# Performance work log

Measured on AMD Instinct MI355X. Metric: run time of the kernel, lower is better.

The kernel has to match this reference:

```python
import jax, jax.numpy as jnp
import numpy as np

HIDDEN = 2048
NUM_HEADS = 16
HEAD_DIM = HIDDEN // NUM_HEADS  # 128
LAYER_IDX = 0


def setup_inputs() -> dict:
    key = jax.random.key(0)
    k1, k2, k3, k4, k5 = jax.random.split(key, 5)
    B, S = 2, 2048
    hidden_states = jax.random.normal(k1, (B, S, HIDDEN), dtype=jnp.float32)
    # causal mask, broadcastable to attn shape (B, Q, H, K)
    causal = jnp.tril(jnp.ones((S, S), dtype=jnp.bool_))  # [Q, K]
    attention_mask = causal[None, :, None, :]  # [1, Q, 1, K]
    c_attn_w = jax.random.normal(k2, (HIDDEN, HIDDEN + 2 * HEAD_DIM), dtype=jnp.float32) * 0.02
    c_attn_b = jax.random.normal(k3, (HIDDEN + 2 * HEAD_DIM,), dtype=jnp.float32) * 0.02
    c_proj_w = jax.random.normal(k4, (HIDDEN, HIDDEN), dtype=jnp.float32) * 0.02
    c_proj_b = jax.random.normal(k5, (HIDDEN,), dtype=jnp.float32) * 0.02
    return {
        "hidden_states": hidden_states,
        "attention_mask": attention_mask,
        "c_attn_w": c_attn_w,
        "c_attn_b": c_attn_b,
        "c_proj_w": c_proj_w,
        "c_proj_b": c_proj_b,
    }


def reference(hidden_states, attention_mask, c_attn_w, c_attn_b, c_proj_w, c_proj_b):
    B, S, D = hidden_states.shape
    H, hd = NUM_HEADS, HEAD_DIM
    # c_attn then split into per-head query and shared (MQA) key/value
    qkv = hidden_states @ c_attn_w + c_attn_b  # [B, S, D + 2*hd]
    query = qkv[..., :D].reshape(B, S, H, hd)  # [B, Q, H, hd]
    k = qkv[..., D:D + hd]                     # [B, K, hd] shared across heads
    v = qkv[..., D + hd:]                      # [B, K, hd]
    # fp32 input => upcast=False => unscale=1, scale = 1/sqrt(head_dim)
    scale = 1.0 / jnp.sqrt(jnp.float32(hd))
    scores = jnp.einsum('bqhd,bkd->bqhk', query, k) * scale  # [B, Q, H, K]
    mask_value = jnp.finfo(jnp.float32).min
    scores = jnp.where(attention_mask, scores, mask_value)
    attn = jax.nn.softmax(scores, axis=-1)
    attn_output = jnp.einsum('bqhk,bkd->bqhd', attn, v).reshape(B, S, D)
    attn_output = attn_output @ c_proj_w + c_proj_b
    return attn_output
```

## Files before the change

### kernel.cpp

```cpp
#include <hip/hip_runtime.h>
#include <hip/hip_bf16.h>

typedef __bf16 bf16_t;
typedef __bf16 bf16x8 __attribute__((ext_vector_type(8)));
typedef __bf16 bf16x4 __attribute__((ext_vector_type(4)));
typedef float f32x4 __attribute__((ext_vector_type(4)));

#define S_LEN 2048
#define HID   2048
#define NH    16
#define HD    128
#define QKVN  2304
#define NEG_BIG (-30000.0f)

__device__ __forceinline__ void gld_lds16(const bf16_t* g, bf16_t* l) {
  __builtin_amdgcn_global_load_lds(
      (const __attribute__((address_space(1))) void*)((const void*)g),
      (__attribute__((address_space(3))) void*)((void*)l), 16, 0, 0);
}

__global__ __launch_bounds__(256) void cvt_f32_bf16_kernel(
    const float* __restrict__ in, bf16_t* __restrict__ out, int n)
{
  int i = (blockIdx.x * 256 + threadIdx.x) * 4;
  if (i < n) {
    float4 v = *(const float4*)(in + i);
    bf16x4 o;
    o[0] = (bf16_t)v.x; o[1] = (bf16_t)v.y; o[2] = (bf16_t)v.z; o[3] = (bf16_t)v.w;
    *(bf16x4*)(out + i) = o;
  }
}

__global__ __launch_bounds__(256) void transpose_cvt_kernel(
    const float* __restrict__ in, bf16_t* __restrict__ out, int K, int N)
{
  int nc = threadIdx.x & 63;
  int kg = threadIdx.x >> 6;
  int n  = blockIdx.x * 64 + nc;
  int kb = blockIdx.y * 32 + kg * 8;
  bf16x8 v;
  #pragma unroll
  for (int i = 0; i < 8; ++i) v[i] = (bf16_t)in[(size_t)(kb + i) * N + n];
  *(bf16x8*)(out + (size_t)n * K + kb) = v;
}

__global__ __launch_bounds__(256) void vt_extract_kernel(
    const bf16_t* __restrict__ qkv, bf16_t* __restrict__ vtg)
{
  int d  = threadIdx.x & 127;
  int sg = threadIdx.x >> 7;
  int b  = blockIdx.y;
  int s8 = blockIdx.x * 2 + sg;
  bf16x8 v;
  #pragma unroll
  for (int i = 0; i < 8; ++i)
    v[i] = qkv[((size_t)(b * S_LEN + s8 * 8 + i)) * QKVN + HID + HD + d];
  *(bf16x8*)(vtg + ((size_t)(b * HD + d)) * S_LEN + s8 * 8) = v;
}

template <typename OutT>
__global__ __launch_bounds__(256) void gemm_bias_kernel(
    const bf16_t* __restrict__ A, const bf16_t* __restrict__ WT,
    const float* __restrict__ bias, OutT* __restrict__ C,
    int K, int lda, int ldc)
{
  __shared__ bf16_t Ash[128 * 64];
  __shared__ bf16_t Bsh[128 * 64];

  const int tid  = threadIdx.x;
  const int wave = tid >> 6;
  const int lane = tid & 63;
  const int quad = lane >> 4;
  const int c16  = lane & 15;
  const int wm = wave >> 1;
  const int wn = wave & 1;
  const int n0 = blockIdx.x * 128;
  const int m0 = blockIdx.y * 128;

  f32x4 acc[4][4] = {};

  for (int k0 = 0; k0 < K; k0 += 64) {
    __syncthreads();
    #pragma unroll
    for (int j = 0; j < 4; ++j) {
      int cbase = wave * 256 + j * 64;
      int c = cbase + lane;
      int row = c >> 3;
      int kcl = (c ^ row) & 7;
      gld_lds16(A  + (size_t)(m0 + row) * lda + k0 + kcl * 8, Ash + cbase * 8);
      gld_lds16(WT + (size_t)(n0 + row) * K   + k0 + kcl * 8, Bsh + cbase * 8);
    }
    __syncthreads();

    #pragma unroll
    for (int kk = 0; kk < 2; ++kk) {
      bf16x8 af[4], bfr[4];
      #pragma unroll
      for (int rb = 0; rb < 4; ++rb) {
        int row = wm * 64 + rb * 16 + c16;
        int kcp = ((kk * 4 + quad) ^ row) & 7;
        af[rb] = *(const bf16x8*)(Ash + row * 64 + kcp * 8);
      }
      #pragma unroll
      for (int nt = 0; nt < 4; ++nt) {
        int row = wn * 64 + nt * 16 + c16;
        int kcp = ((kk * 4 + quad) ^ row) & 7;
        bfr[nt] = *(const bf16x8*)(Bsh + row * 64 + kcp * 8);
      }
      #pragma unroll
      for (int rb = 0; rb < 4; ++rb)
        #pragma unroll
        for (int nt = 0; nt < 4; ++nt)
          acc[rb][nt] = __builtin_amdgcn_mfma_f32_16x16x32_bf16(af[rb], bfr[nt],
                                                                acc[rb][nt], 0, 0, 0);
    }
  }

  #pragma unroll
  for (int nt = 0; nt < 4; ++nt) {
    int col = n0 + wn * 64 + nt * 16 + c16;
    float bv = bias[col];
    #pragma unroll
    for (int rb = 0; rb < 4; ++rb) {
      int rbase = m0 + wm * 64 + rb * 16 + quad * 4;
      #pragma unroll
      for (int r = 0; r < 4; ++r)
        C[(size_t)(rbase + r) * ldc + col] = (OutT)(acc[rb][nt][r] + bv);
    }
  }
}

__global__ __launch_bounds__(512, 4) void mqa_attn_kernel(
    const bf16_t* __restrict__ qkv, const bf16_t* __restrict__ vtg,
    bf16_t* __restrict__ out)
{
  __shared__ bf16_t Ksh[2][64 * 136];
  __shared__ bf16_t VTsh[2][128 * 72];

  const int tid  = threadIdx.x;
  const int wave = tid >> 6;
  const int g    = wave >> 2;
  const int wv   = wave & 3;
  const int lane = tid & 63;
  const int quad = lane >> 4;
  const int c16  = lane & 15;
  const int gt   = tid & 255;
  const int h = blockIdx.y;
  const int b = blockIdx.z;
  const float qscale = 0.08838834764831845f * 1.4426950408889634f;

  const bf16_t* kbase = qkv + (size_t)b * S_LEN * QKVN + HID;
  const bf16_t* vtb   = vtg + (size_t)b * HD * S_LEN;

  for (int half = 0; half < 2; ++half) {
    const int qb = half ? (31 - (int)blockIdx.x) : (int)blockIdx.x;
    const int q0 = qb * 64;
    const int qrow = q0 + wv * 16 + c16;

    const bf16_t* qp = qkv + ((size_t)(b * S_LEN + qrow)) * QKVN + h * HD;
    bf16x8 qf[4];
    #pragma unroll
    for (int ks = 0; ks < 4; ++ks) {
      bf16x8 t = *(const bf16x8*)(qp + ks * 32 + quad * 8);
      #pragma unroll
      for (int j = 0; j < 8; ++j) t[j] = (bf16_t)((float)t[j] * qscale);
      qf[ks] = t;
    }

    float m_q = NEG_BIG, l_q = 0.0f;
    f32x4 o[8] = {};
    const int nss = (qb + 2) >> 1;

    for (int ss = 0; ss < nss; ++ss) {
      const int kt = 2 * ss + g;
      const bool active = (kt <= qb);

      __syncthreads();
      if (active) {
        for (int c = gt; c < 1024; c += 256) {
          int key = c >> 4, dc = c & 15;
          *(bf16x8*)(&Ksh[g][key * 136 + dc * 8]) =
              *(const bf16x8*)(kbase + (size_t)(kt * 64 + key) * QKVN + dc * 8);
        }
        for (int c = gt; c < 1024; c += 256) {
          int d = c >> 3, kc = c & 7;
          *(bf16x8*)(&VTsh[g][d * 72 + kc * 8]) =
              *(const bf16x8*)(vtb + (size_t)d * S_LEN + kt * 64 + kc * 8);
        }
      }
      __syncthreads();

      float p[4][4];
      if (active) {
        f32x4 sacc[4] = {};
        #pragma unroll
        for (int mt = 0; mt < 4; ++mt) {
          #pragma unroll
          for (int ks = 0; ks < 4; ++ks) {
            bf16x8 kf = *(const bf16x8*)(&Ksh[g][(mt * 16 + c16) * 136 + ks * 32 + quad * 8]);
            sacc[mt] = __builtin_amdgcn_mfma_f32_16x16x32_bf16(kf, qf[ks], sacc[mt], 0, 0, 0);
          }
        }
        float mx = NEG_BIG;
        if (kt == qb) {
          #pragma unroll
          for (int mt = 0; mt < 4; ++mt) {
            #pragma unroll
            for (int r = 0; r < 4; ++r) {
              int key = kt * 64 + mt * 16 + quad * 4 + r;
              float v = sacc[mt][r];
              if (key > qrow) v = NEG_BIG;
              p[mt][r] = v;
              mx = fmaxf(mx, v);
            }
          }
        } else {
          #pragma unroll
          for (int mt = 0; mt < 4; ++mt) {
            #pragma unroll
            for (int r = 0; r < 4; ++r) {
              p[mt][r] = sacc[mt][r];
              mx = fmaxf(mx, sacc[mt][r]);
            }
          }
        }
        mx = fmaxf(mx, __shfl_xor(mx, 16));
        mx = fmaxf(mx, __shfl_xor(mx, 32));

        float mn = fmaxf(m_q, mx);
        float alpha = __builtin_exp2f(m_q - mn);
        m_q = mn;

        float rs = 0.f;
        #pragma unroll
        for (int mt = 0; mt < 4; ++mt) {
          #pragma unroll
          for (int r = 0; r < 4; ++r) {
            float pe = __builtin_exp2f(p[mt][r] - m_q);
            p[mt][r] = pe;
            rs += pe;
          }
        }
        rs += __shfl_xor(rs, 16);
        rs += __shfl_xor(rs, 32);
        l_q = l_q * alpha + rs;
        #pragma unroll
        for (int mt8 = 0; mt8 < 8; ++mt8) {
          #pragma unroll
          for (int r = 0; r < 4; ++r) o[mt8][r] *= alpha;
        }
      }

      __syncthreads();
      if (active) {
        bf16_t* Pw = &Ksh[g][(wv * 16) * 136];
        #pragma unroll
        for (int mt = 0; mt < 4; ++mt) {
          bf16x4 pk;
          #pragma unroll
          for (int r = 0; r < 4; ++r) pk[r] = (bf16_t)p[mt][r];
          *(bf16x4*)(Pw + c16 * 136 + mt * 16 + quad * 4) = pk;
        }
        bf16x8 pf[2];
        #pragma unroll
        for (int kh = 0; kh < 2; ++kh)
          pf[kh] = *(const bf16x8*)(Pw + c16 * 136 + kh * 32 + quad * 8);
        #pragma unroll
        for (int mt8 = 0; mt8 < 8; ++mt8) {
          #pragma unroll
          for (int kh = 0; kh < 2; ++kh) {
            bf16x8 vf = *(const bf16x8*)(&VTsh[g][(mt8 * 16 + c16) * 72 + kh * 32 + quad * 8]);
            o[mt8] = __builtin_amdgcn_mfma_f32_16x16x32_bf16(vf, pf[kh], o[mt8], 0, 0, 0);
          }
        }
      }
    }

    __syncthreads();
    float* scr = (float*)&VTsh[0][0];
    float* mls = scr + 4 * 16 * 132;
    if (g == 1) {
      float* op = scr + (wv * 16 + c16) * 132;
      #pragma unroll
      for (int mt8 = 0; mt8 < 8; ++mt8)
        *(f32x4*)(op + mt8 * 16 + quad * 4) = o[mt8];
      if (quad == 0) {
        mls[wv * 32 + c16] = m_q;
        mls[wv * 32 + 16 + c16] = l_q;
      }
    }
    __syncthreads();
    if (g == 0) {
      float m1 = mls[wv * 32 + c16];
      float l1 = mls[wv * 32 + 16 + c16];
      float mF = fmaxf(m_q, m1);
      float a0 = __builtin_exp2f(m_q - mF);
      float a1 = __builtin_exp2f(m1 - mF);
      float inv = 1.0f / fmaxf(a0 * l_q + a1 * l1, 1e-20f);
      a0 *= inv; a1 *= inv;
      const float* op = scr + (wv * 16 + c16) * 132;
      bf16_t* Osh = &Ksh[0][(wv * 16) * 136];
      #pragma unroll
      for (int mt8 = 0; mt8 < 8; ++mt8) {
        f32x4 o1 = *(const f32x4*)(op + mt8 * 16 + quad * 4);
        bf16x4 pk;
        #pragma unroll
        for (int r = 0; r < 4; ++r) pk[r] = (bf16_t)(o[mt8][r] * a0 + o1[r] * a1);
        *(bf16x4*)(Osh + c16 * 136 + mt8 * 16 + quad * 4) = pk;
      }
      int ql = lane >> 2, dc = lane & 3;
      #pragma unroll
      for (int i = 0; i < 4; ++i) {
        bf16x8 v = *(const bf16x8*)(Osh + ql * 136 + dc * 8 + i * 32);
        *(bf16x8*)(out + ((size_t)(b * S_LEN + q0 + wv * 16 + ql)) * HID
                       + h * HD + dc * 8 + i * 32) = v;
      }
    }
  }
}

extern "C" void kernel_launch(void* const* d_in, const int* in_sizes, int n_in,
                              void* d_out, int out_size, void* d_ws, size_t ws_size,
                              hipStream_t stream) {
  const float* hidden_f   = (const float*)d_in[0];
  const float* c_attn_w_f = (const float*)d_in[2];
  const float* c_attn_b_f = (const float*)d_in[3];
  const float* c_proj_w_f = (const float*)d_in[4];
  const float* c_proj_b_f = (const float*)d_in[5];
  float* out = (float*)d_out;

  const int M = 2 * S_LEN;
  const int nH  = M * HID;
  const int nWq = HID * QKVN;
  const int nWp = HID * HID;

  bf16_t* hbf   = (bf16_t*)d_ws;
  bf16_t* wqT   = hbf  + nH;
  bf16_t* wpT   = wqT  + nWq;
  bf16_t* qkv   = wpT  + nWp;
  bf16_t* attn  = qkv  + (size_t)M * QKVN;
  bf16_t* vtg   = attn + (size_t)M * HID;

  cvt_f32_bf16_kernel<<<nH / 1024, 256, 0, stream>>>(hidden_f, hbf, nH);
  dim3 gt1(QKVN / 64, HID / 32);
  transpose_cvt_kernel<<<gt1, 256, 0, stream>>>(c_attn_w_f, wqT, HID, QKVN);
  dim3 gt2(HID / 64, HID / 32);
  transpose_cvt_kernel<<<gt2, 256, 0, stream>>>(c_proj_w_f, wpT, HID, HID);

  dim3 g1(QKVN / 128, M / 128);
  gemm_bias_kernel<bf16_t><<<g1, 256, 0, stream>>>(hbf, wqT, c_attn_b_f, qkv,
                                                   HID, HID, QKVN);

  dim3 gv(S_LEN / 16, 2);
  vt_extract_kernel<<<gv, 256, 0, stream>>>(qkv, vtg);

  dim3 g2(16, NH, 2);
  mqa_attn_kernel<<<g2, 512, 0, stream>>>(qkv, vtg, attn);

  dim3 g3(HID / 128, M / 128);
  gemm_bias_kernel<float><<<g3, 256, 0, stream>>>(attn, wpT, c_proj_b_f, out,
                                                  HID, HID, HID);
}
```

Before: 340.1 us.

## Prefetch next K/V tile into registers and skip softmax rescale below threshold

Loads the next K and V^T tile into registers while the current tile is computed, so global load latency overlaps with MFMA and softmax work. Index math for the copies is hoisted out of the loop. The online-softmax rescale of the output accumulator is now done only when the running max grows by more than a threshold, which removes per-tile multiplies of the accumulator. The cost is extra register pressure from the prefetch buffers, and unnormalised exponentials that can reach up to 2^8.

```diff
diff --git a/kernel.cpp b/kernel.cpp
--- a/kernel.cpp
+++ b/kernel.cpp
@@ -12,6 +12,7 @@
 #define HD    128
 #define QKVN  2304
 #define NEG_BIG (-30000.0f)
+#define RESCALE_THR 8.0f
 
 __device__ __forceinline__ void gld_lds16(const bf16_t* g, bf16_t* l) {
   __builtin_amdgcn_global_load_lds(
@@ -152,6 +153,14 @@
   const bf16_t* kbase = qkv + (size_t)b * S_LEN * QKVN + HID;
   const bf16_t* vtb   = vtg + (size_t)b * HD * S_LEN;
 
+  int kkey[4], kdcB[4], vdd[4], vkcB[4];
+  #pragma unroll
+  for (int i = 0; i < 4; ++i) {
+    int c = gt + i * 256;
+    kkey[i] = c >> 4;  kdcB[i] = (c & 15) * 8;
+    vdd[i]  = c >> 3;  vkcB[i] = (c & 7) * 8;
+  }
+
   for (int half = 0; half < 2; ++half) {
     const int qb = half ? (31 - (int)blockIdx.x) : (int)blockIdx.x;
     const int q0 = qb * 64;
@@ -171,21 +180,37 @@
     f32x4 o[8] = {};
     const int nss = (qb + 2) >> 1;
 
+    bf16x8 kpre[4], vpre[4];
+    if (g <= qb) {
+      int kb = g * 64;
+      #pragma unroll
+      for (int i = 0; i < 4; ++i) {
+        kpre[i] = *(const bf16x8*)(kbase + (size_t)(kb + kkey[i]) * QKVN + kdcB[i]);
+        vpre[i] = *(const bf16x8*)(vtb + (size_t)vdd[i] * S_LEN + kb + vkcB[i]);
+      }
+    }
+
     for (int ss = 0; ss < nss; ++ss) {
       const int kt = 2 * ss + g;
       const bool active = (kt <= qb);
 
       __syncthreads();
       if (active) {
-        for (int c = gt; c < 1024; c += 256) {
-          int key = c >> 4, dc = c & 15;
-          *(bf16x8*)(&Ksh[g][key * 136 + dc * 8]) =
-              *(const bf16x8*)(kbase + (size_t)(kt * 64 + key) * QKVN + dc * 8);
-        }
-        for (int c = gt; c < 1024; c += 256) {
-          int d = c >> 3, kc = c & 7;
-          *(bf16x8*)(&VTsh[g][d * 72 + kc * 8]) =
-              *(const bf16x8*)(vtb + (size_t)d * S_LEN + kt * 64 + kc * 8);
+        #pragma unroll
+        for (int i = 0; i < 4; ++i) {
+          *(bf16x8*)(&Ksh[g][kkey[i] * 136 + kdcB[i]])  = kpre[i];
+          *(bf16x8*)(&VTsh[g][vdd[i] * 72 + vkcB[i]])   = vpre[i];
+        }
+      }
+      {
+        int ktn = kt + 2;
+        if (ktn <= qb) {
+          int kb = ktn * 64;
+          #pragma unroll
+          for (int i = 0; i < 4; ++i) {
+            kpre[i] = *(const bf16x8*)(kbase + (size_t)(kb + kkey[i]) * QKVN + kdcB[i]);
+            vpre[i] = *(const bf16x8*)(vtb + (size_t)vdd[i] * S_LEN + kb + vkcB[i]);
+          }
         }
       }
       __syncthreads();
@@ -227,9 +252,17 @@
         mx = fmaxf(mx, __shfl_xor(mx, 16));
         mx = fmaxf(mx, __shfl_xor(mx, 32));
 
-        float mn = fmaxf(m_q, mx);
-        float alpha = __builtin_exp2f(m_q - mn);
-        m_q = mn;
+        if (__any(mx > m_q + RESCALE_THR)) {
+          float mn = fmaxf(m_q, mx);
+          float alpha = __builtin_exp2f(m_q - mn);
+          m_q = mn;
+          l_q *= alpha;
+          #pragma unroll
+          for (int mt8 = 0; mt8 < 8; ++mt8) {
+            #pragma unroll
+            for (int r = 0; r < 4; ++r) o[mt8][r] *= alpha;
+          }
+        }
 
         float rs = 0.f;
         #pragma unroll
@@ -243,12 +276,7 @@
         }
         rs += __shfl_xor(rs, 16);
         rs += __shfl_xor(rs, 32);
-        l_q = l_q * alpha + rs;
-        #pragma unroll
-        for (int mt8 = 0; mt8 < 8; ++mt8) {
-          #pragma unroll
-          for (int r = 0; r < 4; ++r) o[mt8][r] *= alpha;
-        }
+        l_q += rs;
       }
 
       __syncthreads();
```

Result: slower. 385.3 us (+13.3%).
